# Kernel optimization log

Hardware: AMD Instinct MI355X
Metric: run time of the kernel (lower is better)

## Reference

```python
import jax, jax.numpy as jnp
import numpy as np

N_NODES = 8192
N_FEAT = 256
N_EDGES = 131072
K = 4


def setup_inputs() -> dict:
    key = jax.random.key(0)
    k1, k2, k3 = jax.random.split(key, 3)
    x = jax.random.normal(k1, (N_NODES, N_FEAT), dtype=jnp.float32)
    edge_index = jax.random.randint(k2, (2, N_EDGES), 0, N_NODES, dtype=jnp.int64)
    edge_weight = jax.random.uniform(k3, (N_EDGES,), dtype=jnp.float32)
    return {"k": K, "x": x, "edge_index": edge_index, "edge_weight": edge_weight}


def reference(k, x, edge_index, edge_weight):
    n = x.shape[0]
    src, dst = edge_index[0], edge_index[1]
    # Symmetrized dense adjacency, matching the torch loop:
    #   adj[src, dst] = w  then  adj[dst, src] += w
    adj = jnp.zeros((n, n), dtype=x.dtype)
    adj = adj.at[src, dst].set(edge_weight)
    adj = adj.at[dst, src].add(edge_weight)
    # M = [I | A | A^2 | ... | A^{k-1}] (N x kN) times block_diag(x,...,x)
    # (kN x kF) is exactly concat([A^j @ x for j in 0..k-1], axis=1) -- we
    # compute that directly and never form the block-diagonal zeros.
    outs = [x]
    h = x
    for _ in range(1, k):
        h = adj @ h  # A^j @ x  (A symmetric, so order is immaterial)
        outs.append(h)
    return jnp.concatenate(outs, axis=1)  # [N, k*F]
```

## Files before the change

### kernel.cpp

```cpp
#include <hip/hip_runtime.h>

#define N_NODES 8192
#define N_FEAT  256
#define N_EDGES 131072
#define KPOW    4
#define OUT_LD  1024
#define RCAP    128
#define COL_MASK 8191u

typedef float    f32x4 __attribute__((ext_vector_type(4)));
typedef unsigned u32x4 __attribute__((ext_vector_type(4)));
typedef unsigned u32x2 __attribute__((ext_vector_type(2)));

static __device__ __forceinline__ float bflo(unsigned u) {
    union { unsigned i; float f; } v; v.i = u << 16; return v.f;
}
static __device__ __forceinline__ float bfhi(unsigned u) {
    union { unsigned i; float f; } v; v.i = u & 0xffff0000u; return v.f;
}
static __device__ __forceinline__ unsigned short f2bf(float f) {
    union { float f; unsigned i; } v = { f };
    return (unsigned short)((v.i + 0x7fffu + ((v.i >> 16) & 1u)) >> 16);
}

__global__ void k_scatter_copy(const int* __restrict__ ei, const float* __restrict__ ew,
                               int* __restrict__ len, u32x2* __restrict__ ent,
                               const float* __restrict__ x, float* __restrict__ out,
                               unsigned short* __restrict__ xb) {
    if (blockIdx.x < 2048) {
        int t = blockIdx.x * blockDim.x + threadIdx.x;
        int row = t >> 6;
        int lane = t & 63;
        f32x4 v = *(const f32x4*)(x + (size_t)row * N_FEAT + lane * 4);
        *(f32x4*)(out + (size_t)row * OUT_LD + lane * 4) = v;
        u32x2 pb;
        pb.x = ((unsigned)f2bf(v.y) << 16) | f2bf(v.x);
        pb.y = ((unsigned)f2bf(v.w) << 16) | f2bf(v.z);
        *(u32x2*)(xb + (size_t)row * N_FEAT + lane * 4) = pb;
    } else {
        int e = (blockIdx.x - 2048) * blockDim.x + threadIdx.x;
        if (e >= N_EDGES) return;
        int src = ei[e];
        int dst = ei[N_EDGES + e];
        unsigned wbits = __float_as_uint(ew[e]);
        int s0 = atomicAdd(&len[dst], 1);
        if (s0 < RCAP) {
            u32x2 v; v.x = (unsigned)src; v.y = wbits;
            ent[(size_t)dst * RCAP + s0] = v;
        }
        int s1 = atomicAdd(&len[src], 1);
        if (s1 < RCAP) {
            u32x2 v; v.x = (1u << 30) | ((unsigned)e << 13) | (unsigned)dst; v.y = wbits;
            ent[(size_t)src * RCAP + s1] = v;
        }
    }
}

__global__ __launch_bounds__(256) void k_dedup(const int* __restrict__ len,
                                               unsigned* __restrict__ entw) {
    int lane = threadIdx.x & 63;
    int row = blockIdx.x * 4 + (threadIdx.x >> 6);
    int n = __builtin_amdgcn_readfirstlane(len[row]);
    if (n > RCAP) n = RCAP;
    size_t base = (size_t)row * RCAP;
    unsigned v0 = entw[2 * (base + lane)];
    unsigned v1 = entw[2 * (base + 64 + lane)];
    bool k0 = false, k1 = false;
    int j0 = n < 64 ? n : 64;
    for (int j = 0; j < j0; ++j) {
        unsigned b = (unsigned)__shfl((int)v0, j);
        if (b >> 30) {
            k0 |= (((b ^ v0) & COL_MASK) == 0u) && (b > v0);
            k1 |= (((b ^ v1) & COL_MASK) == 0u) && (b > v1);
        }
    }
    for (int j = 0; j < n - 64; ++j) {
        unsigned b = (unsigned)__shfl((int)v1, j);
        if (b >> 30) {
            k0 |= (((b ^ v0) & COL_MASK) == 0u) && (b > v0);
            k1 |= (((b ^ v1) & COL_MASK) == 0u) && (b > v1);
        }
    }
    int ngs = 16 * ((n + 15) >> 4);
    int s1 = 64 + lane;
    if (lane < n) { if (k0 && (v0 >> 30)) entw[2 * (base + lane) + 1] = 0u; }
    else if (lane < ngs) entw[2 * (base + lane) + 1] = 0u;
    if (s1 < n) { if (k1 && (v1 >> 30)) entw[2 * (base + s1) + 1] = 0u; }
    else if (s1 < ngs) entw[2 * (base + s1) + 1] = 0u;
}

__global__ __launch_bounds__(256) void k_spmm(const int* __restrict__ len,
                                              const u32x2* __restrict__ ent,
                                              const unsigned short* __restrict__ hinb,
                                              float* __restrict__ hout,
                                              unsigned short* __restrict__ houtb,
                                              int write_bf) {
    __shared__ u32x2 sent[4 * RCAP];
    int wave = threadIdx.x >> 6;
    int lane = threadIdx.x & 63;
    int row = blockIdx.x * 4 + wave;
    int n = __builtin_amdgcn_readfirstlane(len[row]);
    if (n > RCAP) n = RCAP;

    const u32x2* ep = ent + (size_t)row * RCAP;
    u32x2* sp = sent + wave * RCAP;
    sp[lane] = ep[lane];
    sp[lane + 64] = ep[lane + 64];
    __builtin_amdgcn_s_waitcnt(0);

    int half = lane >> 5;
    int fl   = lane & 31;
    const unsigned short* hbase = hinb + fl * 8;
    float a0 = 0.f, a1 = 0.f, a2 = 0.f, a3 = 0.f,
          a4 = 0.f, a5 = 0.f, a6 = 0.f, a7 = 0.f;
    int ng = (n + 15) >> 4;

    for (int g = 0; g < ng; ++g) {
        const u32x2* ge = sp + g * 16 + half;
        u32x4 us[8];
#pragma unroll
        for (int t = 0; t < 8; ++t) {
            unsigned c = ge[2 * t].x & COL_MASK;
            us[t] = *(const u32x4*)(hbase + (size_t)c * N_FEAT);
        }
#pragma unroll
        for (int t = 0; t < 8; ++t) {
            float w = __uint_as_float(ge[2 * t].y);
            a0 += w * bflo(us[t].x); a1 += w * bfhi(us[t].x);
            a2 += w * bflo(us[t].y); a3 += w * bfhi(us[t].y);
            a4 += w * bflo(us[t].z); a5 += w * bfhi(us[t].z);
            a6 += w * bflo(us[t].w); a7 += w * bfhi(us[t].w);
        }
    }

    a0 += __shfl_xor(a0, 32); a1 += __shfl_xor(a1, 32);
    a2 += __shfl_xor(a2, 32); a3 += __shfl_xor(a3, 32);
    a4 += __shfl_xor(a4, 32); a5 += __shfl_xor(a5, 32);
    a6 += __shfl_xor(a6, 32); a7 += __shfl_xor(a7, 32);

    if (half == 0) {
        float* op = hout + (size_t)row * OUT_LD + fl * 8;
        f32x4 r0; r0.x = a0; r0.y = a1; r0.z = a2; r0.w = a3;
        f32x4 r1; r1.x = a4; r1.y = a5; r1.z = a6; r1.w = a7;
        *(f32x4*)op = r0;
        *(f32x4*)(op + 4) = r1;
    } else if (write_bf) {
        u32x4 pb;
        pb.x = ((unsigned)f2bf(a1) << 16) | f2bf(a0);
        pb.y = ((unsigned)f2bf(a3) << 16) | f2bf(a2);
        pb.z = ((unsigned)f2bf(a5) << 16) | f2bf(a4);
        pb.w = ((unsigned)f2bf(a7) << 16) | f2bf(a6);
        *(u32x4*)(houtb + (size_t)row * N_FEAT + fl * 8) = pb;
    }
}

extern "C" void kernel_launch(void* const* d_in, const int* in_sizes, int n_in,
                              void* d_out, int out_size, void* d_ws, size_t ws_size,
                              hipStream_t stream) {
    const float* x  = (const float*)d_in[1];
    const int*   ei = (const int*)d_in[2];
    const float* ew = (const float*)d_in[3];
    float* out = (float*)d_out;

    int* len   = (int*)d_ws;
    u32x2* ent = (u32x2*)(len + N_NODES);
    unsigned short* hb0 = (unsigned short*)(ent + (size_t)N_NODES * RCAP);
    unsigned short* hb1 = hb0 + (size_t)N_NODES * N_FEAT;
    unsigned short* hb2 = hb1 + (size_t)N_NODES * N_FEAT;

    (void)hipMemsetAsync(len, 0, (size_t)N_NODES * sizeof(int), stream);

    const int TB = 256;
    const int EB = N_EDGES / TB;

    k_scatter_copy<<<2048 + EB, TB, 0, stream>>>(ei, ew, len, ent, x, out, hb0);
    k_dedup<<<N_NODES / 4, TB, 0, stream>>>(len, (unsigned*)ent);

    const unsigned short* hin = hb0;
    for (int j = 1; j < KPOW; ++j) {
        float* hout = out + (size_t)j * N_FEAT;
        unsigned short* houtb = (j == 1) ? hb1 : hb2;
        int write_bf = (j < KPOW - 1) ? 1 : 0;
        k_spmm<<<N_NODES / 4, TB, 0, stream>>>(len, ent, hin, hout, houtb, write_bf);
        hin = houtb;
    }
}
```

Measured before the change: 139.6 us.

## Fuse edge dedup into first SpMM pass and add nontemporal memory hints

Removes the separate dedup kernel and performs duplicate-edge detection inside the first SpMM launch, writing zeroed weights back to global memory for later hops. Padding weights are now masked in registers on each launch rather than stored. Streaming loads and stores of the input, the edge arrays and the fp32 output use nontemporal hints to reduce cache pollution. The first SpMM becomes heavier and its shuffle loop may lengthen that launch.

```diff
diff --git a/kernel.cpp b/kernel.cpp
--- a/kernel.cpp
+++ b/kernel.cpp
@@ -31,8 +31,8 @@
         int t = blockIdx.x * blockDim.x + threadIdx.x;
         int row = t >> 6;
         int lane = t & 63;
-        f32x4 v = *(const f32x4*)(x + (size_t)row * N_FEAT + lane * 4);
-        *(f32x4*)(out + (size_t)row * OUT_LD + lane * 4) = v;
+        f32x4 v = __builtin_nontemporal_load((const f32x4*)(x + (size_t)row * N_FEAT + lane * 4));
+        __builtin_nontemporal_store(v, (f32x4*)(out + (size_t)row * OUT_LD + lane * 4));
         u32x2 pb;
         pb.x = ((unsigned)f2bf(v.y) << 16) | f2bf(v.x);
         pb.y = ((unsigned)f2bf(v.w) << 16) | f2bf(v.z);
@@ -40,9 +40,9 @@
     } else {
         int e = (blockIdx.x - 2048) * blockDim.x + threadIdx.x;
         if (e >= N_EDGES) return;
-        int src = ei[e];
-        int dst = ei[N_EDGES + e];
-        unsigned wbits = __float_as_uint(ew[e]);
+        int src = __builtin_nontemporal_load(ei + e);
+        int dst = __builtin_nontemporal_load(ei + N_EDGES + e);
+        unsigned wbits = __float_as_uint(__builtin_nontemporal_load(ew + e));
         int s0 = atomicAdd(&len[dst], 1);
         if (s0 < RCAP) {
             u32x2 v; v.x = (unsigned)src; v.y = wbits;
@@ -56,45 +56,13 @@
     }
 }
 
-__global__ __launch_bounds__(256) void k_dedup(const int* __restrict__ len,
-                                               unsigned* __restrict__ entw) {
-    int lane = threadIdx.x & 63;
-    int row = blockIdx.x * 4 + (threadIdx.x >> 6);
-    int n = __builtin_amdgcn_readfirstlane(len[row]);
-    if (n > RCAP) n = RCAP;
-    size_t base = (size_t)row * RCAP;
-    unsigned v0 = entw[2 * (base + lane)];
-    unsigned v1 = entw[2 * (base + 64 + lane)];
-    bool k0 = false, k1 = false;
-    int j0 = n < 64 ? n : 64;
-    for (int j = 0; j < j0; ++j) {
-        unsigned b = (unsigned)__shfl((int)v0, j);
-        if (b >> 30) {
-            k0 |= (((b ^ v0) & COL_MASK) == 0u) && (b > v0);
-            k1 |= (((b ^ v1) & COL_MASK) == 0u) && (b > v1);
-        }
-    }
-    for (int j = 0; j < n - 64; ++j) {
-        unsigned b = (unsigned)__shfl((int)v1, j);
-        if (b >> 30) {
-            k0 |= (((b ^ v0) & COL_MASK) == 0u) && (b > v0);
-            k1 |= (((b ^ v1) & COL_MASK) == 0u) && (b > v1);
-        }
-    }
-    int ngs = 16 * ((n + 15) >> 4);
-    int s1 = 64 + lane;
-    if (lane < n) { if (k0 && (v0 >> 30)) entw[2 * (base + lane) + 1] = 0u; }
-    else if (lane < ngs) entw[2 * (base + lane) + 1] = 0u;
-    if (s1 < n) { if (k1 && (v1 >> 30)) entw[2 * (base + s1) + 1] = 0u; }
-    else if (s1 < ngs) entw[2 * (base + s1) + 1] = 0u;
-}
-
 __global__ __launch_bounds__(256) void k_spmm(const int* __restrict__ len,
-                                              const u32x2* __restrict__ ent,
+                                              const u32x2* ent,
+                                              unsigned* entw,
                                               const unsigned short* __restrict__ hinb,
                                               float* __restrict__ hout,
                                               unsigned short* __restrict__ houtb,
-                                              int write_bf) {
+                                              int write_bf, int dedup) {
     __shared__ u32x2 sent[4 * RCAP];
     int wave = threadIdx.x >> 6;
     int lane = threadIdx.x & 63;
@@ -104,8 +72,41 @@
 
     const u32x2* ep = ent + (size_t)row * RCAP;
     u32x2* sp = sent + wave * RCAP;
-    sp[lane] = ep[lane];
-    sp[lane + 64] = ep[lane + 64];
+    u32x2 e0 = __builtin_nontemporal_load(ep + lane);
+    u32x2 e1 = __builtin_nontemporal_load(ep + 64 + lane);
+    if (lane >= n)      e0.y = 0u;
+    if (lane + 64 >= n) e1.y = 0u;
+
+    if (dedup) {
+        unsigned v0 = e0.x, v1 = e1.x;
+        bool k0 = false, k1 = false;
+        int j0 = n < 64 ? n : 64;
+        for (int j = 0; j < j0; ++j) {
+            unsigned b = (unsigned)__shfl((int)v0, j);
+            if (b >> 30) {
+                k0 |= (((b ^ v0) & COL_MASK) == 0u) && (b > v0);
+                k1 |= (((b ^ v1) & COL_MASK) == 0u) && (b > v1);
+            }
+        }
+        for (int j = 0; j < n - 64; ++j) {
+            unsigned b = (unsigned)__shfl((int)v1, j);
+            if (b >> 30) {
+                k0 |= (((b ^ v0) & COL_MASK) == 0u) && (b > v0);
+                k1 |= (((b ^ v1) & COL_MASK) == 0u) && (b > v1);
+            }
+        }
+        size_t wbase = (size_t)row * RCAP * 2;
+        if (lane < n && k0 && (v0 >> 30)) {
+            e0.y = 0u; entw[wbase + 2 * lane + 1] = 0u;
+        }
+        int s1 = lane + 64;
+        if (s1 < n && k1 && (v1 >> 30)) {
+            e1.y = 0u; entw[wbase + 2 * s1 + 1] = 0u;
+        }
+    }
+
+    sp[lane] = e0;
+    sp[lane + 64] = e1;
     __builtin_amdgcn_s_waitcnt(0);
 
     int half = lane >> 5;
@@ -142,8 +143,8 @@
         float* op = hout + (size_t)row * OUT_LD + fl * 8;
         f32x4 r0; r0.x = a0; r0.y = a1; r0.z = a2; r0.w = a3;
         f32x4 r1; r1.x = a4; r1.y = a5; r1.z = a6; r1.w = a7;
-        *(f32x4*)op = r0;
-        *(f32x4*)(op + 4) = r1;
+        __builtin_nontemporal_store(r0, (f32x4*)op);
+        __builtin_nontemporal_store(r1, (f32x4*)(op + 4));
     } else if (write_bf) {
         u32x4 pb;
         pb.x = ((unsigned)f2bf(a1) << 16) | f2bf(a0);
@@ -174,14 +175,15 @@
     const int EB = N_EDGES / TB;
 
     k_scatter_copy<<<2048 + EB, TB, 0, stream>>>(ei, ew, len, ent, x, out, hb0);
-    k_dedup<<<N_NODES / 4, TB, 0, stream>>>(len, (unsigned*)ent);
 
     const unsigned short* hin = hb0;
     for (int j = 1; j < KPOW; ++j) {
         float* hout = out + (size_t)j * N_FEAT;
         unsigned short* houtb = (j == 1) ? hb1 : hb2;
         int write_bf = (j < KPOW - 1) ? 1 : 0;
-        k_spmm<<<N_NODES / 4, TB, 0, stream>>>(len, ent, hin, hout, houtb, write_bf);
+        int dedup    = (j == 1) ? 1 : 0;
+        k_spmm<<<N_NODES / 4, TB, 0, stream>>>(len, ent, (unsigned*)ent, hin,
+                                               hout, houtb, write_bf, dedup);
         hin = houtb;
     }
 }
```

New measurement: 134.9 us. 3.3% less time.
